# Optimization experiments

Measured on AMD Instinct MI355X. Metric: run time of the kernel, lower is better.

Reference implementation:

```python
import jax, jax.numpy as jnp
import numpy as np


def _graph_conv(x, src, dst, W_rel, b_rel, W_root):
    # PyG GraphConv (aggr='add'): out = lin_rel(sum_{j->i} x_j) + lin_root(x_i)
    agg = jax.ops.segment_sum(x[src], dst, num_segments=x.shape[0])  # [N, d]
    return agg @ W_rel + b_rel + x @ W_root


def setup_inputs() -> dict:
    N, E, D, H, G = 50000, 800000, 128, 128, 256
    key = jax.random.key(0)
    ks = jax.random.split(key, 24)
    x = jax.random.normal(ks[0], (N, D), dtype=jnp.float32)
    edge_index = jax.random.randint(ks[1], (2, E), 0, N, dtype=jnp.int64)
    batch = jnp.sort(jax.random.randint(ks[2], (N,), 0, G, dtype=jnp.int64))
    inp = {"x": x, "edge_index": edge_index, "batch": batch, "num_graphs": G}
    dims = [(D, H), (H, H), (H, H), (H, H), (H, H)]
    for i, (din, dout) in enumerate(dims, 1):
        s = 1.0 / np.sqrt(din)
        inp[f"W_rel{i}"] = jax.random.normal(ks[3 * i], (din, dout), dtype=jnp.float32) * s
        inp[f"b_rel{i}"] = jax.random.normal(ks[3 * i + 1], (dout,), dtype=jnp.float32) * s
        inp[f"W_root{i}"] = jax.random.normal(ks[3 * i + 2], (din, dout), dtype=jnp.float32) * s
    inp["fc1_W"] = jax.random.normal(ks[18], (H, H), dtype=jnp.float32) / np.sqrt(H)
    inp["fc1_b"] = jax.random.normal(ks[19], (H,), dtype=jnp.float32) / np.sqrt(H)
    inp["fc2_W"] = jax.random.normal(ks[20], (H, 1), dtype=jnp.float32) / np.sqrt(H)
    inp["fc2_b"] = jax.random.normal(ks[21], (1,), dtype=jnp.float32) / np.sqrt(H)
    return inp


def reference(x, edge_index, batch, num_graphs,
              W_rel1, b_rel1, W_root1,
              W_rel2, b_rel2, W_root2,
              W_rel3, b_rel3, W_root3,
              W_rel4, b_rel4, W_root4,
              W_rel5, b_rel5, W_root5,
              fc1_W, fc1_b, fc2_W, fc2_b):
    src, dst = edge_index[0], edge_index[1]
    h = x
    for Wr, br, Wl in ((W_rel1, b_rel1, W_root1), (W_rel2, b_rel2, W_root2),
                       (W_rel3, b_rel3, W_root3), (W_rel4, b_rel4, W_root4),
                       (W_rel5, b_rel5, W_root5)):
        h = jax.nn.relu(_graph_conv(h, src, dst, Wr, br, Wl))
    # global_add_pool -> [num_graphs, H]
    g = jax.ops.segment_sum(h, batch, num_segments=num_graphs)
    g = jax.nn.relu(g @ fc1_W + fc1_b)
    # dropout is identity in eval mode
    return g @ fc2_W + fc2_b  # [num_graphs, 1]
```

## Files before the change

### kernel.cpp

```cpp
#include <hip/hip_runtime.h>
#include <hip/hip_bf16.h>

typedef __attribute__((ext_vector_type(4))) float f32x4;
typedef __attribute__((ext_vector_type(8))) _Float16 f16x8;
typedef __attribute__((ext_vector_type(4))) _Float16 f16x4;

#define CHUNK 4096
#define BSH 7
#define CAP 4096

__global__ __launch_bounds__(256) void cvt_kernel(const float* __restrict__ x,
                                                  _Float16* __restrict__ h, int total4) {
  int i = blockIdx.x * blockDim.x + threadIdx.x;
  if (i < total4) {
    float4 v = *(const float4*)(x + (size_t)i * 4);
    f16x4 o = {(_Float16)v.x, (_Float16)v.y, (_Float16)v.z, (_Float16)v.w};
    *(f16x4*)(h + (size_t)i * 4) = o;
  }
}

__global__ __launch_bounds__(256) void bhist_kernel(const int* __restrict__ dst,
                                                    int* __restrict__ gcnt, int E, int nb) {
  __shared__ int l[512];
  int t = threadIdx.x;
  for (int i = t; i < 512; i += 256) l[i] = 0;
  __syncthreads();
  int cbase = blockIdx.x * CHUNK;
  #pragma unroll
  for (int i = 0; i < CHUNK / 256; ++i) {
    int idx = cbase + i * 256 + t;
    if (idx < E) atomicAdd(&l[dst[idx] >> BSH], 1);
  }
  __syncthreads();
  for (int i = t; i < nb; i += 256) {
    int c = l[i];
    if (c) atomicAdd(&gcnt[i], c);
  }
}

__global__ __launch_bounds__(512) void bscan_kernel(const int* __restrict__ gcnt,
                                                    int* __restrict__ base,
                                                    int* __restrict__ gcursor, int nb, int E) {
  __shared__ int wsum[8], wpre[8];
  int t = threadIdx.x, lane = t & 63, w = t >> 6;
  int v = (t < nb) ? gcnt[t] : 0;
  int incl = v;
  #pragma unroll
  for (int o = 1; o < 64; o <<= 1) {
    int x = __shfl_up(incl, o, 64);
    if (lane >= o) incl += x;
  }
  if (lane == 63) wsum[w] = incl;
  __syncthreads();
  if (t == 0) {
    int run = 0;
    #pragma unroll
    for (int q = 0; q < 8; ++q) { wpre[q] = run; run += wsum[q]; }
  }
  __syncthreads();
  int excl = wpre[w] + incl - v;
  if (t < nb) { base[t] = excl; gcursor[t] = excl; }
  if (t == 0) base[nb] = E;
}

__global__ __launch_bounds__(256) void bscatter_kernel(const int* __restrict__ src,
                                                       const int* __restrict__ dst,
                                                       int* __restrict__ gcursor,
                                                       int2* __restrict__ pairs, int E, int nb) {
  __shared__ int lcnt[512], lstart[512], lpos[512], lgbase[512];
  __shared__ int2 lp[CHUNK];
  __shared__ int wsum[4], wpre[4];
  int t = threadIdx.x, lane = t & 63, w = t >> 6;
  for (int i = t; i < 512; i += 256) lcnt[i] = 0;
  __syncthreads();
  int cbase = blockIdx.x * CHUNK;
  int m = E - cbase; if (m > CHUNK) m = CHUNK;
  #pragma unroll
  for (int i = 0; i < CHUNK / 256; ++i) {
    int idx = i * 256 + t;
    if (idx < m) atomicAdd(&lcnt[dst[cbase + idx] >> BSH], 1);
  }
  __syncthreads();
  int c0 = lcnt[2 * t], c1 = lcnt[2 * t + 1];
  int s = c0 + c1, incl = s;
  #pragma unroll
  for (int o = 1; o < 64; o <<= 1) {
    int x = __shfl_up(incl, o, 64);
    if (lane >= o) incl += x;
  }
  if (lane == 63) wsum[w] = incl;
  __syncthreads();
  if (t == 0) {
    int run = 0;
    #pragma unroll
    for (int q = 0; q < 4; ++q) { wpre[q] = run; run += wsum[q]; }
  }
  __syncthreads();
  int excl = wpre[w] + incl - s;
  lstart[2 * t] = excl;          lpos[2 * t] = excl;
  lstart[2 * t + 1] = excl + c0; lpos[2 * t + 1] = excl + c0;
  if (2 * t < nb && c0 > 0) lgbase[2 * t] = atomicAdd(&gcursor[2 * t], c0);
  if (2 * t + 1 < nb && c1 > 0) lgbase[2 * t + 1] = atomicAdd(&gcursor[2 * t + 1], c1);
  __syncthreads();
  #pragma unroll
  for (int i = 0; i < CHUNK / 256; ++i) {
    int idx = i * 256 + t;
    if (idx < m) {
      int d = dst[cbase + idx], sv = src[cbase + idx];
      int p = atomicAdd(&lpos[d >> BSH], 1);
      lp[p] = make_int2(sv, d);
    }
  }
  __syncthreads();
  for (int i = t; i < m; i += 256) {
    int2 pr = lp[i];
    int b = pr.y >> BSH;
    pairs[lgbase[b] + (i - lstart[b])] = pr;
  }
}

__global__ __launch_bounds__(256) void bbuild_kernel(const int2* __restrict__ pairs,
                                                     const int* __restrict__ base,
                                                     int* __restrict__ row_ptr,
                                                     int* __restrict__ col, int N, int E) {
  __shared__ int cnt[128], cur[128], w2[2];
  __shared__ int cl[CAP];
  int b = blockIdx.x, t = threadIdx.x;
  int mb = base[b], me = base[b + 1], m = me - mb;
  if (t < 128) cnt[t] = 0;
  __syncthreads();
  for (int i = t; i < m; i += 256) atomicAdd(&cnt[pairs[mb + i].y & 127], 1);
  __syncthreads();
  int v = 0, incl = 0;
  if (t < 128) {
    v = cnt[t]; incl = v;
    #pragma unroll
    for (int o = 1; o < 64; o <<= 1) {
      int x = __shfl_up(incl, o, 64);
      if ((t & 63) >= o) incl += x;
    }
    if ((t & 63) == 63) w2[t >> 6] = incl;
  }
  __syncthreads();
  if (t < 128) {
    int excl = incl - v + ((t & 64) ? w2[0] : 0);
    cur[t] = excl;
    int node = (b << BSH) + t;
    if (node < N) row_ptr[node] = mb + excl;
  }
  if (b == 0 && t == 0) row_ptr[N] = E;
  __syncthreads();
  if (m <= CAP) {
    for (int i = t; i < m; i += 256) {
      int2 p = pairs[mb + i];
      int pos = atomicAdd(&cur[p.y & 127], 1);
      cl[pos] = p.x;
    }
    __syncthreads();
    for (int i = t; i < m; i += 256) col[mb + i] = cl[i];
  } else {
    for (int i = t; i < m; i += 256) {
      int2 p = pairs[mb + i];
      int pos = atomicAdd(&cur[p.y & 127], 1);
      col[mb + pos] = p.x;
    }
  }
}

struct W10 { const float* p[10]; };

__global__ __launch_bounds__(256) void prep_kernel(W10 wp, _Float16* __restrict__ Whi,
                                                   _Float16* __restrict__ Wlo, float wscale) {
  int l = blockIdx.x >> 7;
  int idx = (blockIdx.x & 127) * 256 + threadIdx.x;
  int col = idx >> 8;
  int k = idx & 255;
  const float* __restrict__ Wrel = wp.p[l];
  const float* __restrict__ Wroot = wp.p[5 + l];
  float v = (k < 128) ? Wrel[k * 128 + col] : Wroot[(k - 128) * 128 + col];
  v *= wscale;
  _Float16 hi = (_Float16)v;
  _Float16 lo = (_Float16)(v - (float)hi);
  Whi[(size_t)l * 32768 + idx] = hi;
  Wlo[(size_t)l * 32768 + idx] = lo;
}

__global__ __launch_bounds__(256) void spmm_kernel(const _Float16* __restrict__ hin,
                                                   const int* __restrict__ row_ptr,
                                                   const int* __restrict__ col,
                                                   _Float16* __restrict__ agg, int N) {
  int t = threadIdx.x;
  int grp = t >> 4, l16 = t & 15;
  int row = blockIdx.x * 16 + grp;
  if (row >= N) return;
  const char* __restrict__ hb = (const char*)hin;
  unsigned lofs = (unsigned)l16 << 4;
  int s = row_ptr[row], e = row_ptr[row + 1];
  float acc[8];
  #pragma unroll
  for (int q = 0; q < 8; ++q) acc[q] = 0.f;
  if (s < e) {
    int c[8];
    #pragma unroll
    for (int q = 0; q < 8; ++q) { int x = s + q; c[q] = col[x < e ? x : e - 1]; }
    int i = s;
    for (; i + 8 <= e; i += 8) {
      f16x8 v[8];
      #pragma unroll
      for (int q = 0; q < 8; ++q) v[q] = *(const f16x8*)(hb + ((((unsigned)c[q]) << 8) | lofs));
      #pragma unroll
      for (int q = 0; q < 8; ++q) { int x = i + 8 + q; c[q] = col[x < e ? x : e - 1]; }
      #pragma unroll
      for (int z = 0; z < 8; ++z)
        acc[z] += (((float)v[0][z] + (float)v[1][z]) + ((float)v[2][z] + (float)v[3][z])) +
                  (((float)v[4][z] + (float)v[5][z]) + ((float)v[6][z] + (float)v[7][z]));
    }
    if (i < e) {
      f16x8 v[8];
      #pragma unroll
      for (int q = 0; q < 8; ++q) v[q] = *(const f16x8*)(hb + ((((unsigned)c[q]) << 8) | lofs));
      #pragma unroll
      for (int q = 0; q < 8; ++q) {
        float m = (i + q < e) ? 1.f : 0.f;
        #pragma unroll
        for (int z = 0; z < 8; ++z) acc[z] = fmaf(m, (float)v[q][z], acc[z]);
      }
    }
  }
  f16x8 o;
  #pragma unroll
  for (int q = 0; q < 8; ++q) o[q] = (_Float16)acc[q];
  *(f16x8*)(agg + (size_t)row * 128 + l16 * 8) = o;
}

__global__ __launch_bounds__(256) void gemm_kernel(const _Float16* __restrict__ Aagg,
                                                   const _Float16* __restrict__ Ah,
                                                   const _Float16* __restrict__ Whi,
                                                   const _Float16* __restrict__ Wlo,
                                                   const float* __restrict__ bias,
                                                   float bscale,
                                                   _Float16* __restrict__ out, int N) {
  int wv = threadIdx.x >> 6;
  int lane = threadIdx.x & 63;
  int l16 = lane & 15;
  int khalf = lane >> 4;
  int koff = khalf * 8;
  int row_base = blockIdx.x * 64;
  int col_base = wv * 32;

  f32x4 acc[4][2];
  #pragma unroll
  for (int r = 0; r < 4; r++)
    #pragma unroll
    for (int c = 0; c < 2; c++) acc[r][c] = (f32x4){0.f, 0.f, 0.f, 0.f};

  #pragma unroll
  for (int ks = 0; ks < 8; ++ks) {
    int k0 = ks * 32;
    const _Float16* Abase = (ks < 4) ? (Aagg + k0) : (Ah + (k0 - 128));
    f16x8 bh[2], bl[2];
    #pragma unroll
    for (int c = 0; c < 2; c++) {
      int col = col_base + c * 16 + l16;
      bh[c] = *(const f16x8*)(Whi + col * 256 + k0 + koff);
      bl[c] = *(const f16x8*)(Wlo + col * 256 + k0 + koff);
    }
    #pragma unroll
    for (int r = 0; r < 4; r++) {
      int row = row_base + r * 16 + l16;
      if (row >= N) row = N - 1;
      f16x8 a = *(const f16x8*)(Abase + (size_t)row * 128 + koff);
      #pragma unroll
      for (int c = 0; c < 2; c++) {
        acc[r][c] = __builtin_amdgcn_mfma_f32_16x16x32_f16(a, bh[c], acc[r][c], 0, 0, 0);
        acc[r][c] = __builtin_amdgcn_mfma_f32_16x16x32_f16(a, bl[c], acc[r][c], 0, 0, 0);
      }
    }
  }

  #pragma unroll
  for (int r = 0; r < 4; r++) {
    #pragma unroll
    for (int c = 0; c < 2; c++) {
      int col = col_base + c * 16 + l16;
      float b = bias[col] * bscale;
      #pragma unroll
      for (int tt = 0; tt < 4; tt++) {
        int row = row_base + r * 16 + khalf * 4 + tt;
        if (row < N) {
          float v = acc[r][c][tt] + b;
          out[(size_t)row * 128 + col] = (_Float16)(v > 0.f ? v : 0.f);
        }
      }
    }
  }
}

static __device__ __forceinline__ int lbound(const int* __restrict__ a, int n, int v) {
  int lo = 0, hi = n;
  while (lo < hi) {
    int m = (lo + hi) >> 1;
    if (a[m] < v) lo = m + 1; else hi = m;
  }
  return lo;
}

__global__ __launch_bounds__(128) void poolhead_kernel(const _Float16* __restrict__ h,
                                                       const int* __restrict__ batch,
                                                       const float* __restrict__ fc1W,
                                                       const float* __restrict__ fc1b,
                                                       const float* __restrict__ fc2W,
                                                       const float* __restrict__ fc2b,
                                                       float* __restrict__ out, int N,
                                                       float unscale) {
  int gid = blockIdx.x, j = threadIdx.x;
  int start = lbound(batch, N, gid);
  int end = lbound(batch, N, gid + 1);
  float acc = 0.f;
  int r = start;
  for (; r + 3 < end; r += 4) {
    acc += (float)h[(size_t)r * 128 + j] + (float)h[(size_t)(r + 1) * 128 + j] +
           (float)h[(size_t)(r + 2) * 128 + j] + (float)h[(size_t)(r + 3) * 128 + j];
  }
  for (; r < end; ++r) acc += (float)h[(size_t)r * 128 + j];
  __shared__ float grow[128];
  __shared__ float red[128];
  grow[j] = acc * unscale;
  __syncthreads();
  float a1 = fc1b[j];
  #pragma unroll 8
  for (int k = 0; k < 128; ++k) a1 = fmaf(grow[k], fc1W[k * 128 + j], a1);
  a1 = a1 > 0.f ? a1 : 0.f;
  red[j] = a1 * fc2W[j];
  __syncthreads();
  #pragma unroll
  for (int s2 = 64; s2 > 0; s2 >>= 1) {
    if (j < s2) red[j] += red[j + s2];
    __syncthreads();
  }
  if (j == 0) out[gid] = red[0] + fc2b[0];
}

extern "C" void kernel_launch(void* const* d_in, const int* in_sizes, int n_in,
                              void* d_out, int out_size, void* d_ws, size_t ws_size,
                              hipStream_t stream) {
  const float* x = (const float*)d_in[0];
  const int* edge = (const int*)d_in[1];
  const int* batch = (const int*)d_in[2];
  const int N = in_sizes[0] / 128;
  const int E = in_sizes[1] / 2;
  const int G = out_size;
  const int* esrc = edge;
  const int* edst = edge + E;
  const int NB = (N + 127) >> BSH;

  char* ws = (char*)d_ws;
  size_t off = 0;
  auto alloc = [&](size_t bytes) -> void* {
    void* p = ws + off;
    off = (off + bytes + 255) & ~(size_t)255;
    return p;
  };
  _Float16* x16  = (_Float16*)alloc((size_t)N * 128 * 2);
  _Float16* bufA = (_Float16*)alloc((size_t)N * 128 * 2);
  _Float16* bufB = (_Float16*)alloc((size_t)N * 128 * 2);
  _Float16* agg  = (_Float16*)alloc((size_t)N * 128 * 2);
  _Float16* Whi  = (_Float16*)alloc((size_t)5 * 32768 * 2);
  _Float16* Wlo  = (_Float16*)alloc((size_t)5 * 32768 * 2);
  int* row_ptr   = (int*)alloc((size_t)(N + 1) * 4);
  int* col       = (int*)alloc((size_t)E * 4);
  int2* pairs    = (int2*)alloc((size_t)E * 8);
  int* gcnt      = (int*)alloc(512 * 4);
  int* base      = (int*)alloc(520 * 4);
  int* gcursor   = (int*)alloc(512 * 4);
  if (off > ws_size) return;

  hipMemsetAsync(gcnt, 0, 512 * 4, stream);

  int nb1 = (E + CHUNK - 1) / CHUNK;
  bhist_kernel<<<nb1, 256, 0, stream>>>(edst, gcnt, E, NB);
  bscan_kernel<<<1, 512, 0, stream>>>(gcnt, base, gcursor, NB, E);
  bscatter_kernel<<<nb1, 256, 0, stream>>>(esrc, edst, gcursor, pairs, E, NB);
  bbuild_kernel<<<NB, 256, 0, stream>>>(pairs, base, row_ptr, col, N, E);

  cvt_kernel<<<(N * 128 / 4 + 255) / 256, 256, 0, stream>>>(x, x16, N * 128 / 4);

  const float S = 8.0f;
  W10 wp;
  for (int l = 0; l < 5; ++l) {
    wp.p[l] = (const float*)d_in[4 + 3 * l];
    wp.p[5 + l] = (const float*)d_in[6 + 3 * l];
  }
  prep_kernel<<<640, 256, 0, stream>>>(wp, Whi, Wlo, 1.0f / S);

  const _Float16* hin = x16;
  _Float16* hout = bufA;
  int spmm_grid = (N + 15) / 16;
  int gemm_grid = (N + 63) / 64;
  float bscale = 1.0f;
  for (int l = 0; l < 5; ++l) {
    bscale /= S;
    spmm_kernel<<<spmm_grid, 256, 0, stream>>>(hin, row_ptr, col, agg, N);
    gemm_kernel<<<gemm_grid, 256, 0, stream>>>(agg, hin,
                                               Whi + (size_t)l * 32768, Wlo + (size_t)l * 32768,
                                               (const float*)d_in[5 + 3 * l], bscale, hout, N);
    hin = hout;
    hout = (hout == bufA) ? bufB : bufA;
  }
  poolhead_kernel<<<G, 128, 0, stream>>>(hin, batch,
                                         (const float*)d_in[19], (const float*)d_in[20],
                                         (const float*)d_in[21], (const float*)d_in[22],
                                         (float*)d_out, N, 32768.0f);
}
```

Before: 374.4 us.

## Split node features into four column planes and process SpMM per plane

Feature matrices are stored as four planes of 32 fp16 columns each, and SpMM runs one pass per plane so every gather reads a compact 64-byte row slice. The aim is a per-pass working set (about 3.2 MB per plane) that fits in cache, so random neighbour gathers hit L2 or MALL instead of HBM. GEMM, conversion and pooling are adjusted to the planar layout. Separately, the bucket histogram writes per-block counts that the scan kernel reduces, which removes the memset and the global atomics. The cost is four times as many passes over row_ptr and col.

After: 372.1 us, median of 2. No clear change (-0.6%).

```diff
diff --git a/kernel.cpp b/kernel.cpp
--- a/kernel.cpp
+++ b/kernel.cpp
@@ -9,18 +9,21 @@
 #define BSH 7
 #define CAP 4096
 
+
 __global__ __launch_bounds__(256) void cvt_kernel(const float* __restrict__ x,
-                                                  _Float16* __restrict__ h, int total4) {
+                                                  _Float16* __restrict__ hp, int N) {
   int i = blockIdx.x * blockDim.x + threadIdx.x;
-  if (i < total4) {
-    float4 v = *(const float4*)(x + (size_t)i * 4);
+  if (i < N * 32) {
+    int r = i >> 5, jg = i & 31;
+    float4 v = *(const float4*)(x + (size_t)r * 128 + jg * 4);
     f16x4 o = {(_Float16)v.x, (_Float16)v.y, (_Float16)v.z, (_Float16)v.w};
-    *(f16x4*)(h + (size_t)i * 4) = o;
+    int plane = jg >> 3, wc = (jg & 7) * 4;
+    *(f16x4*)(hp + (size_t)plane * N * 32 + (size_t)r * 32 + wc) = o;
   }
 }
 
 __global__ __launch_bounds__(256) void bhist_kernel(const int* __restrict__ dst,
-                                                    int* __restrict__ gcnt, int E, int nb) {
+                                                    int* __restrict__ blkhist, int E, int nb) {
   __shared__ int l[512];
   int t = threadIdx.x;
   for (int i = t; i < 512; i += 256) l[i] = 0;
@@ -32,18 +35,20 @@
     if (idx < E) atomicAdd(&l[dst[idx] >> BSH], 1);
   }
   __syncthreads();
-  for (int i = t; i < nb; i += 256) {
-    int c = l[i];
-    if (c) atomicAdd(&gcnt[i], c);
-  }
-}
-
-__global__ __launch_bounds__(512) void bscan_kernel(const int* __restrict__ gcnt,
+  for (int i = t; i < 512; i += 256) blkhist[blockIdx.x * 512 + i] = l[i];
+}
+
+__global__ __launch_bounds__(512) void bscan_kernel(const int* __restrict__ blkhist, int nblk,
                                                     int* __restrict__ base,
                                                     int* __restrict__ gcursor, int nb, int E) {
   __shared__ int wsum[8], wpre[8];
   int t = threadIdx.x, lane = t & 63, w = t >> 6;
-  int v = (t < nb) ? gcnt[t] : 0;
+  int v = 0;
+  int b = 0;
+  for (; b + 4 <= nblk; b += 4)
+    v += blkhist[b * 512 + t] + blkhist[(b + 1) * 512 + t] +
+         blkhist[(b + 2) * 512 + t] + blkhist[(b + 3) * 512 + t];
+  for (; b < nblk; ++b) v += blkhist[b * 512 + t];
   int incl = v;
   #pragma unroll
   for (int o = 1; o < 64; o <<= 1) {
@@ -185,16 +190,20 @@
   Wlo[(size_t)l * 32768 + idx] = lo;
 }
 
-__global__ __launch_bounds__(256) void spmm_kernel(const _Float16* __restrict__ hin,
+__global__ __launch_bounds__(256) void spmm_kernel(const _Float16* __restrict__ hplanes,
                                                    const int* __restrict__ row_ptr,
                                                    const int* __restrict__ col,
-                                                   _Float16* __restrict__ agg, int N) {
+                                                   _Float16* __restrict__ aggplanes,
+                                                   int N, int nbpp) {
+  int pass = blockIdx.x / nbpp;
+  int blk = blockIdx.x - pass * nbpp;
   int t = threadIdx.x;
-  int grp = t >> 4, l16 = t & 15;
-  int row = blockIdx.x * 16 + grp;
+  int quad = t >> 2, lq = t & 3;
+  int row = blk * 64 + quad;
   if (row >= N) return;
-  const char* __restrict__ hb = (const char*)hin;
-  unsigned lofs = (unsigned)l16 << 4;
+  size_t planeN = (size_t)N * 32;
+  const char* __restrict__ hb = (const char*)(hplanes + (size_t)pass * planeN);
+  unsigned lofs = (unsigned)lq << 4;
   int s = row_ptr[row], e = row_ptr[row + 1];
   float acc[8];
   #pragma unroll
@@ -207,7 +216,7 @@
     for (; i + 8 <= e; i += 8) {
       f16x8 v[8];
       #pragma unroll
-      for (int q = 0; q < 8; ++q) v[q] = *(const f16x8*)(hb + ((((unsigned)c[q]) << 8) | lofs));
+      for (int q = 0; q < 8; ++q) v[q] = *(const f16x8*)(hb + ((((unsigned)c[q]) << 6) | lofs));
       #pragma unroll
       for (int q = 0; q < 8; ++q) { int x = i + 8 + q; c[q] = col[x < e ? x : e - 1]; }
       #pragma unroll
@@ -218,7 +227,7 @@
     if (i < e) {
       f16x8 v[8];
       #pragma unroll
-      for (int q = 0; q < 8; ++q) v[q] = *(const f16x8*)(hb + ((((unsigned)c[q]) << 8) | lofs));
+      for (int q = 0; q < 8; ++q) v[q] = *(const f16x8*)(hb + ((((unsigned)c[q]) << 6) | lofs));
       #pragma unroll
       for (int q = 0; q < 8; ++q) {
         float m = (i + q < e) ? 1.f : 0.f;
@@ -230,16 +239,17 @@
   f16x8 o;
   #pragma unroll
   for (int q = 0; q < 8; ++q) o[q] = (_Float16)acc[q];
-  *(f16x8*)(agg + (size_t)row * 128 + l16 * 8) = o;
-}
-
-__global__ __launch_bounds__(256) void gemm_kernel(const _Float16* __restrict__ Aagg,
-                                                   const _Float16* __restrict__ Ah,
+  *(f16x8*)(aggplanes + (size_t)pass * planeN + (size_t)row * 32 + lq * 8) = o;
+}
+
+__global__ __launch_bounds__(256) void gemm_kernel(const _Float16* __restrict__ aggp,
+                                                   const _Float16* __restrict__ hp,
                                                    const _Float16* __restrict__ Whi,
                                                    const _Float16* __restrict__ Wlo,
                                                    const float* __restrict__ bias,
                                                    float bscale,
-                                                   _Float16* __restrict__ out, int N) {
+                                                   _Float16* __restrict__ outp, int N) {
+  size_t planeN = (size_t)N * 32;
   int wv = threadIdx.x >> 6;
   int lane = threadIdx.x & 63;
   int l16 = lane & 15;
@@ -257,7 +267,8 @@
   #pragma unroll
   for (int ks = 0; ks < 8; ++ks) {
     int k0 = ks * 32;
-    const _Float16* Abase = (ks < 4) ? (Aagg + k0) : (Ah + (k0 - 128));
+    const _Float16* Abase = (ks < 4) ? (aggp + (size_t)ks * planeN)
+                                     : (hp + (size_t)(ks - 4) * planeN);
     f16x8 bh[2], bl[2];
     #pragma unroll
     for (int c = 0; c < 2; c++) {
@@ -269,7 +280,7 @@
     for (int r = 0; r < 4; r++) {
       int row = row_base + r * 16 + l16;
       if (row >= N) row = N - 1;
-      f16x8 a = *(const f16x8*)(Abase + (size_t)row * 128 + koff);
+      f16x8 a = *(const f16x8*)(Abase + (size_t)row * 32 + koff);
       #pragma unroll
       for (int c = 0; c < 2; c++) {
         acc[r][c] = __builtin_amdgcn_mfma_f32_16x16x32_f16(a, bh[c], acc[r][c], 0, 0, 0);
@@ -282,14 +293,15 @@
   for (int r = 0; r < 4; r++) {
     #pragma unroll
     for (int c = 0; c < 2; c++) {
-      int col = col_base + c * 16 + l16;
-      float b = bias[col] * bscale;
+      int cc = col_base + c * 16 + l16;
+      float b = bias[cc] * bscale;
       #pragma unroll
       for (int tt = 0; tt < 4; tt++) {
         int row = row_base + r * 16 + khalf * 4 + tt;
         if (row < N) {
           float v = acc[r][c][tt] + b;
-          out[(size_t)row * 128 + col] = (_Float16)(v > 0.f ? v : 0.f);
+          outp[(size_t)wv * planeN + (size_t)row * 32 + (c * 16 + l16)] =
+              (_Float16)(v > 0.f ? v : 0.f);
         }
       }
     }
@@ -316,13 +328,15 @@
   int gid = blockIdx.x, j = threadIdx.x;
   int start = lbound(batch, N, gid);
   int end = lbound(batch, N, gid + 1);
+  size_t planeN = (size_t)N * 32;
+  const _Float16* __restrict__ base = h + (size_t)(j >> 5) * planeN + (j & 31);
   float acc = 0.f;
   int r = start;
   for (; r + 3 < end; r += 4) {
-    acc += (float)h[(size_t)r * 128 + j] + (float)h[(size_t)(r + 1) * 128 + j] +
-           (float)h[(size_t)(r + 2) * 128 + j] + (float)h[(size_t)(r + 3) * 128 + j];
-  }
-  for (; r < end; ++r) acc += (float)h[(size_t)r * 128 + j];
+    acc += (float)base[(size_t)r * 32] + (float)base[(size_t)(r + 1) * 32] +
+           (float)base[(size_t)(r + 2) * 32] + (float)base[(size_t)(r + 3) * 32];
+  }
+  for (; r < end; ++r) acc += (float)base[(size_t)r * 32];
   __shared__ float grow[128];
   __shared__ float red[128];
   grow[j] = acc * unscale;
@@ -353,6 +367,7 @@
   const int* esrc = edge;
   const int* edst = edge + E;
   const int NB = (N + 127) >> BSH;
+  const int nb1 = (E + CHUNK - 1) / CHUNK;
 
   char* ws = (char*)d_ws;
   size_t off = 0;
@@ -370,20 +385,17 @@
   int* row_ptr   = (int*)alloc((size_t)(N + 1) * 4);
   int* col       = (int*)alloc((size_t)E * 4);
   int2* pairs    = (int2*)alloc((size_t)E * 8);
-  int* gcnt      = (int*)alloc(512 * 4);
+  int* blkhist   = (int*)alloc((size_t)nb1 * 512 * 4);
   int* base      = (int*)alloc(520 * 4);
   int* gcursor   = (int*)alloc(512 * 4);
   if (off > ws_size) return;
 
-  hipMemsetAsync(gcnt, 0, 512 * 4, stream);
-
-  int nb1 = (E + CHUNK - 1) / CHUNK;
-  bhist_kernel<<<nb1, 256, 0, stream>>>(edst, gcnt, E, NB);
-  bscan_kernel<<<1, 512, 0, stream>>>(gcnt, base, gcursor, NB, E);
+  bhist_kernel<<<nb1, 256, 0, stream>>>(edst, blkhist, E, NB);
+  bscan_kernel<<<1, 512, 0, stream>>>(blkhist, nb1, base, gcursor, NB, E);
   bscatter_kernel<<<nb1, 256, 0, stream>>>(esrc, edst, gcursor, pairs, E, NB);
   bbuild_kernel<<<NB, 256, 0, stream>>>(pairs, base, row_ptr, col, N, E);
 
-  cvt_kernel<<<(N * 128 / 4 + 255) / 256, 256, 0, stream>>>(x, x16, N * 128 / 4);
+  cvt_kernel<<<(N * 32 + 255) / 256, 256, 0, stream>>>(x, x16, N);
 
   const float S = 8.0f;
   W10 wp;
@@ -395,12 +407,12 @@
 
   const _Float16* hin = x16;
   _Float16* hout = bufA;
-  int spmm_grid = (N + 15) / 16;
+  int nbpp = (N + 63) / 64;
   int gemm_grid = (N + 63) / 64;
   float bscale = 1.0f;
   for (int l = 0; l < 5; ++l) {
     bscale /= S;
-    spmm_kernel<<<spmm_grid, 256, 0, stream>>>(hin, row_ptr, col, agg, N);
+    spmm_kernel<<<4 * nbpp, 256, 0, stream>>>(hin, row_ptr, col, agg, N, nbpp);
     gemm_kernel<<<gemm_grid, 256, 0, stream>>>(agg, hin,
                                                Whi + (size_t)l * 32768, Wlo + (size_t)l * 32768,
                                                (const float*)d_in[5 + 3 * l], bscale, hout, N);
```
